# Performance work log

Hardware: AMD Instinct MI355X
Metric: run time of the kernel (lower is better)

Reference implementation:

```python
import jax, jax.numpy as jnp
import numpy as np

N_CRIT = 128
N_PAIRS = N_CRIT * (N_CRIT - 1) // 2  # 8128
BATCH = 16384
MIN_W = 1e-07


def setup_inputs() -> dict:
    key = jax.random.key(0)
    k1, k2, k3, k4 = jax.random.split(key, 4)
    x = jax.random.uniform(k1, (BATCH, N_CRIT + N_PAIRS), dtype=jnp.float32)
    # criteria layer weight: init uniform(0.1, 1.0)
    wc = jax.random.uniform(k2, (1, N_CRIT), dtype=jnp.float32, minval=0.1, maxval=1.0)
    # interaction layer weight: init normal(0, 0.1)
    wint = 0.1 * jax.random.normal(k3, (1, N_PAIRS), dtype=jnp.float32)
    thr = jax.random.uniform(k4, (1,), dtype=jnp.float32)
    return {"x": x, "wc": wc, "wint": wint, "thr": thr}


def _constrained_weights(wc, wint):
    # LinearGreaterThanZero.w(): weights < 0 are replaced by MIN_W (in-place .data op)
    wc_eff = jnp.where(wc < 0, MIN_W, wc)
    # LinearInteraction.w(): for each pair (i, j), i < j (row-major upper triangle):
    #   w_ij = max(w_ij, -w_i, -w_j)   -- vectorized over all pairs at once
    ii, jj = jnp.triu_indices(N_CRIT, k=1)  # matches nested-loop order
    lower = jnp.maximum(-wc_eff[:, ii], -wc_eff[:, jj])  # [1, N_PAIRS]
    wint_eff = jnp.maximum(wint, lower)
    return wc_eff, wint_eff


def reference(x, wc, wint, thr):
    wc_eff, wint_eff = _constrained_weights(wc, wint)
    x_wi = x[:, :N_CRIT] @ wc_eff.T          # [B, 1]
    x_wij = x[:, N_CRIT:] @ wint_eff.T       # [B, 1]
    weight_sum = wc_eff.sum() + wint_eff.sum()
    score = (x_wi + x_wij) / weight_sum
    # ThresholdLayer: learnable scalar threshold followed by sigmoid
    return jax.nn.sigmoid(score - thr)
```

## Files before the change

kernel.cpp:

```cpp
#include <hip/hip_runtime.h>
#include <math.h>

#define N_CRIT  128
#define N_PAIRS 8128
#define N_TOT   (N_CRIT + N_PAIRS)
#define N_VEC4  (N_TOT / 4)
#define BATCH   16384
#define MIN_W   1e-7f

__global__ __launch_bounds__(256) void prep_weights(
    const float* __restrict__ wc,
    const float* __restrict__ wint,
    float* __restrict__ w_eff,
    float* __restrict__ wsum)
{
    __shared__ float s_wc[N_CRIT];
    __shared__ float s_part[4];
    const int tid = threadIdx.x;

    float local = 0.0f;
    if (tid < N_CRIT) {
        float v   = wc[tid];
        float eff = (v < 0.0f) ? MIN_W : v;
        s_wc[tid]  = eff;
        w_eff[tid] = eff;
        local += eff;
    }
    __syncthreads();

    for (int p = tid; p < N_PAIRS; p += 256) {
        float disc = 65025.0f - 8.0f * (float)p;
        int i = (int)((255.0f - sqrtf(disc)) * 0.5f);
        if (i < 0) i = 0;
        while (i > 0 && (i * (255 - i)) / 2 > p) --i;
        while (((i + 1) * (254 - i)) / 2 <= p) ++i;
        int j = p - (i * (255 - i)) / 2 + i + 1;
        float lower = fmaxf(-s_wc[i], -s_wc[j]);
        float w = fmaxf(wint[p], lower);
        w_eff[N_CRIT + p] = w;
        local += w;
    }

    #pragma unroll
    for (int off = 32; off > 0; off >>= 1)
        local += __shfl_down(local, off, 64);
    if ((tid & 63) == 0) s_part[tid >> 6] = local;
    __syncthreads();
    if (tid == 0)
        *wsum = s_part[0] + s_part[1] + s_part[2] + s_part[3];
}

__global__ __launch_bounds__(256) void choquet_dot(
    const float* __restrict__ x,
    const float* __restrict__ w_eff,
    const float* __restrict__ wsum,
    const float* __restrict__ thr,
    float* __restrict__ out)
{
    const int row = blockIdx.x;
    const int tid = threadIdx.x;

    const float4* __restrict__ xr = (const float4*)(x + (size_t)row * N_TOT);
    const float4* __restrict__ wv = (const float4*)w_eff;

    float acc = 0.0f;
    for (int c = tid; c < N_VEC4; c += 256) {
        float4 a = xr[c];
        float4 b = wv[c];
        acc = fmaf(a.x, b.x, acc);
        acc = fmaf(a.y, b.y, acc);
        acc = fmaf(a.z, b.z, acc);
        acc = fmaf(a.w, b.w, acc);
    }

    #pragma unroll
    for (int off = 32; off > 0; off >>= 1)
        acc += __shfl_down(acc, off, 64);

    __shared__ float s_part[4];
    if ((tid & 63) == 0) s_part[tid >> 6] = acc;
    __syncthreads();

    if (tid == 0) {
        float dot   = s_part[0] + s_part[1] + s_part[2] + s_part[3];
        float score = dot / (*wsum) - thr[0];
        out[row] = 1.0f / (1.0f + expf(-score));
    }
}

extern "C" void kernel_launch(void* const* d_in, const int* in_sizes, int n_in,
                              void* d_out, int out_size, void* d_ws, size_t ws_size,
                              hipStream_t stream) {
    const float* x    = (const float*)d_in[0];
    const float* wc   = (const float*)d_in[1];
    const float* wint = (const float*)d_in[2];
    const float* thr  = (const float*)d_in[3];
    float* out = (float*)d_out;

    float* w_eff = (float*)d_ws;
    float* wsum  = w_eff + N_TOT;

    prep_weights<<<1, 256, 0, stream>>>(wc, wint, w_eff, wsum);
    choquet_dot<<<BATCH, 256, 0, stream>>>(x, w_eff, wsum, thr, out);
}
```

Baseline: 715.3 us.

## Map one wavefront per row with unrolled nontemporal loads and no block sync

Each 64-lane wavefront now handles a whole row, four rows per block, which removes the shared-memory reduction and __syncthreads. The main loop runs a fixed count, unrolled by 8, with four independent accumulators and a masked tail, and it loads x with nontemporal hints. The weight sum is inverted once in the prep kernel so the epilogue uses an fma and fast __expf. Each wave now issues more loads in flight, but fewer waves cover a given row.

```diff
diff --git a/kernel.cpp b/kernel.cpp
--- a/kernel.cpp
+++ b/kernel.cpp
@@ -5,14 +5,18 @@
 #define N_PAIRS 8128
 #define N_TOT   (N_CRIT + N_PAIRS)
 #define N_VEC4  (N_TOT / 4)
+#define N_FULL  2048
 #define BATCH   16384
 #define MIN_W   1e-7f
+#define ROWS_PER_BLOCK 4
+
+typedef float vf4 __attribute__((ext_vector_type(4)));
 
 __global__ __launch_bounds__(256) void prep_weights(
     const float* __restrict__ wc,
     const float* __restrict__ wint,
     float* __restrict__ w_eff,
-    float* __restrict__ wsum)
+    float* __restrict__ inv_wsum)
 {
     __shared__ float s_wc[N_CRIT];
     __shared__ float s_part[4];
@@ -47,44 +51,53 @@
     if ((tid & 63) == 0) s_part[tid >> 6] = local;
     __syncthreads();
     if (tid == 0)
-        *wsum = s_part[0] + s_part[1] + s_part[2] + s_part[3];
+        *inv_wsum = 1.0f / (s_part[0] + s_part[1] + s_part[2] + s_part[3]);
 }
 
 __global__ __launch_bounds__(256) void choquet_dot(
     const float* __restrict__ x,
     const float* __restrict__ w_eff,
-    const float* __restrict__ wsum,
+    const float* __restrict__ inv_wsum,
     const float* __restrict__ thr,
     float* __restrict__ out)
 {
-    const int row = blockIdx.x;
-    const int tid = threadIdx.x;
+    const int wave = threadIdx.x >> 6;
+    const int lane = threadIdx.x & 63;
+    const int row  = blockIdx.x * ROWS_PER_BLOCK + wave;
 
-    const float4* __restrict__ xr = (const float4*)(x + (size_t)row * N_TOT);
-    const float4* __restrict__ wv = (const float4*)w_eff;
+    const vf4* __restrict__ xr = (const vf4*)(x + (size_t)row * N_TOT);
+    const vf4* __restrict__ wv = (const vf4*)w_eff;
 
-    float acc = 0.0f;
-    for (int c = tid; c < N_VEC4; c += 256) {
-        float4 a = xr[c];
-        float4 b = wv[c];
-        acc = fmaf(a.x, b.x, acc);
-        acc = fmaf(a.y, b.y, acc);
-        acc = fmaf(a.z, b.z, acc);
-        acc = fmaf(a.w, b.w, acc);
+    float a0 = 0.0f, a1 = 0.0f, a2 = 0.0f, a3 = 0.0f;
+
+    #pragma unroll 8
+    for (int it = 0; it < N_FULL / 64; ++it) {
+        const int c = lane + (it << 6);
+        vf4 a = __builtin_nontemporal_load(&xr[c]);
+        vf4 b = wv[c];
+        a0 = fmaf(a.x, b.x, a0);
+        a1 = fmaf(a.y, b.y, a1);
+        a2 = fmaf(a.z, b.z, a2);
+        a3 = fmaf(a.w, b.w, a3);
+    }
+    if (lane < (N_VEC4 - N_FULL)) {
+        const int c = N_FULL + lane;
+        vf4 a = __builtin_nontemporal_load(&xr[c]);
+        vf4 b = wv[c];
+        a0 = fmaf(a.x, b.x, a0);
+        a1 = fmaf(a.y, b.y, a1);
+        a2 = fmaf(a.z, b.z, a2);
+        a3 = fmaf(a.w, b.w, a3);
     }
 
+    float acc = (a0 + a1) + (a2 + a3);
     #pragma unroll
     for (int off = 32; off > 0; off >>= 1)
         acc += __shfl_down(acc, off, 64);
 
-    __shared__ float s_part[4];
-    if ((tid & 63) == 0) s_part[tid >> 6] = acc;
-    __syncthreads();
-
-    if (tid == 0) {
-        float dot   = s_part[0] + s_part[1] + s_part[2] + s_part[3];
-        float score = dot / (*wsum) - thr[0];
-        out[row] = 1.0f / (1.0f + expf(-score));
+    if (lane == 0) {
+        float score = fmaf(acc, inv_wsum[0], -thr[0]);
+        out[row] = 1.0f / (1.0f + __expf(-score));
     }
 }
 
@@ -97,9 +110,9 @@
     const float* thr  = (const float*)d_in[3];
     float* out = (float*)d_out;
 
-    float* w_eff = (float*)d_ws;
-    float* wsum  = w_eff + N_TOT;
+    float* w_eff    = (float*)d_ws;
+    float* inv_wsum = w_eff + N_TOT;
 
-    prep_weights<<<1, 256, 0, stream>>>(wc, wint, w_eff, wsum);
-    choquet_dot<<<BATCH, 256, 0, stream>>>(x, w_eff, wsum, thr, out);
+    prep_weights<<<1, 256, 0, stream>>>(wc, wint, w_eff, inv_wsum);
+    choquet_dot<<<BATCH / ROWS_PER_BLOCK, 256, 0, stream>>>(x, w_eff, inv_wsum, thr, out);
 }
```

New measurement: 685.6 us. -4.2%, faster.
